# Kernel tuning notes

Measured on AMD Instinct MI355X. Metric: run time of the kernel, lower is better.

## Reference

```python
import jax, jax.numpy as jnp
import numpy as np

H = 16
D_MODEL = 1024
D_K = D_MODEL // H
NEG = -1e9


def setup_inputs() -> dict:
    key = jax.random.key(0)
    ks = jax.random.split(key, 12)
    B, S = 2, 2048
    inp = {
        "query": jax.random.normal(ks[0], (B, S, D_MODEL), jnp.float32),
        "key": jax.random.normal(ks[1], (B, S, D_MODEL), jnp.float32),
        "value": jax.random.normal(ks[2], (B, S, D_MODEL), jnp.float32),
        "mask": jnp.ones((B, 1, S), jnp.int32),
    }
    s = 1.0 / np.sqrt(D_MODEL)
    for i, nm in enumerate(["Wq", "Wk", "Wv", "Wo"]):
        inp[nm] = jax.random.normal(ks[3 + i], (D_MODEL, D_MODEL), jnp.float32) * s
        inp["b" + nm[1]] = jax.random.normal(ks[7 + i], (D_MODEL,), jnp.float32) * s
    return inp


def _split_heads(x):
    B, S, _ = x.shape
    return x.reshape(B, S, H, D_K).transpose(0, 2, 1, 3)  # [B,H,S,Dk]


def reference(query, key, value, mask, Wq, bq, Wk, bk, Wv, bv, Wo, bo):
    q = _split_heads(query @ Wq + bq)
    k = _split_heads(key @ Wk + bk)
    v = _split_heads(value @ Wv + bv)
    scores = jnp.einsum("bhqd,bhkd->bhqk", q, k) / jnp.sqrt(jnp.float32(D_K))
    # mask [B,1,Sk] -> broadcast as [B,1,1,Sk]
    scores = jnp.where(mask[:, None, :, :] == 0, NEG, scores)
    attn = jax.nn.softmax(scores, axis=-1)  # dropout is identity in eval mode
    out = jnp.einsum("bhqk,bhkd->bhqd", attn, v)
    B, _, Sq, _ = out.shape
    out = out.transpose(0, 2, 1, 3).reshape(B, Sq, H * D_K)
    return out @ Wo + bo
```

## Files before the change

kernel.cpp:

```cpp
#include <hip/hip_runtime.h>
#include <hip/hip_bf16.h>

typedef __attribute__((ext_vector_type(8))) short short8;
typedef __attribute__((ext_vector_type(4))) float float4v;
typedef __attribute__((ext_vector_type(2))) unsigned int uint2v;
typedef __hip_bfloat16 bf16;

#define MFMA16(a, b, c) __builtin_amdgcn_mfma_f32_16x16x32_bf16((a), (b), (c), 0, 0, 0)

static __device__ __forceinline__ short8 load8(const bf16* p) {
    return *reinterpret_cast<const short8*>(p);
}
static __device__ __forceinline__ unsigned short bfu(float x) {
    union { bf16 b; unsigned short u; } c; c.b = __float2bfloat16(x); return c.u;
}
static __device__ __forceinline__ unsigned pack2(float lo, float hi) {
    return ((unsigned)bfu(hi) << 16) | bfu(lo);
}
static __device__ __forceinline__ short bf_bits(float x) {
    union { bf16 b; short u; } c; c.b = __float2bfloat16(x); return c.u;
}
static __device__ __forceinline__ short8 cvt8(float4 a, float4 b) {
    short8 r;
    r[0] = bf_bits(a.x); r[1] = bf_bits(a.y); r[2] = bf_bits(a.z); r[3] = bf_bits(a.w);
    r[4] = bf_bits(b.x); r[5] = bf_bits(b.y); r[6] = bf_bits(b.z); r[7] = bf_bits(b.w);
    return r;
}

typedef const __attribute__((address_space(1))) unsigned int* gp1;
typedef __attribute__((address_space(3))) unsigned int* lp3;
static __device__ __forceinline__ void async16(const void* g, void* l) {
    __builtin_amdgcn_global_load_lds((gp1)g, (lp3)l, 16, 0, 0);
}

__global__ __launch_bounds__(256) void transpose_qkv(
    const float* __restrict__ Wq, const float* __restrict__ Wk,
    const float* __restrict__ Wv, bf16* __restrict__ out_base)
{
    __shared__ bf16 tile[64][65];
    const float* in = (blockIdx.z == 0) ? Wq : (blockIdx.z == 1) ? Wk : Wv;
    bf16* out = out_base + (size_t)blockIdx.z * 1048576;
    int tx = threadIdx.x, ty = threadIdx.y;
    int bx = blockIdx.x * 64, by = blockIdx.y * 64;
    for (int i = ty; i < 64; i += 4)
        tile[i][tx] = __float2bfloat16(in[(size_t)(by + i) * 1024 + bx + tx]);
    __syncthreads();
    for (int i = ty; i < 64; i += 4)
        out[(size_t)(bx + i) * 1024 + by + tx] = tile[tx][i];
}

__global__ __launch_bounds__(256) void transpose_one(
    const float* __restrict__ in, bf16* __restrict__ out)
{
    __shared__ bf16 tile[64][65];
    int tx = threadIdx.x, ty = threadIdx.y;
    int bx = blockIdx.x * 64, by = blockIdx.y * 64;
    for (int i = ty; i < 64; i += 4)
        tile[i][tx] = __float2bfloat16(in[(size_t)(by + i) * 1024 + bx + tx]);
    __syncthreads();
    for (int i = ty; i < 64; i += 4)
        out[(size_t)(bx + i) * 1024 + by + tx] = tile[tx][i];
}

__global__ __launch_bounds__(256, 3) void qkv_gemm(
    const float* __restrict__ Xq, const float* __restrict__ Xk,
    const float* __restrict__ Xv, const bf16* __restrict__ Wt_all,
    const float* __restrict__ bq, const float* __restrict__ bk,
    const float* __restrict__ bv,
    bf16* __restrict__ outq, bf16* __restrict__ outk, bf16* __restrict__ outv)
{
    __shared__ float As[128 * 64];
    __shared__ bf16  Bs[128 * 64];

    int wg = blockIdx.x;
    int xcd = wg & 7;
    int jj = wg >> 3;
    int grp = xcd * 12 + (jj >> 3);
    int z = grp >> 5;
    int m_blk = grp & 31;
    int n_blk = jj & 7;

    const float* X    = (z == 0) ? Xq : (z == 1) ? Xk : Xv;
    const float* bias = (z == 0) ? bq : (z == 1) ? bk : bv;
    const bf16*  Wt   = Wt_all + (size_t)z * 1048576;
    bf16*        out  = (z == 0) ? outq : (z == 1) ? outk : outv;
    bool vmode = (z == 2);

    int tid = threadIdx.x;
    int w = tid >> 6, lane = tid & 63, l16 = lane & 15, quad = lane >> 4;
    int m_base = m_blk * 128, n_base = n_blk * 128;

    int r4 = lane >> 4, s16 = lane & 15;
    int r8 = lane >> 3, s8 = lane & 7;
    const float* Asrc0 = X + (size_t)(m_base + w * 32 + r4) * 1024 + ((s16 ^ r4) << 2);
    const float* Asrc1 = X + (size_t)(m_base + w * 32 + r4) * 1024 + ((s16 ^ (4 + r4)) << 2);
    const bf16*  Bsrc  = Wt + (size_t)(n_base + w * 32 + r8) * 1024 + ((s8 ^ r8) << 3);

    int wm = (w & 1) * 64, wn = (w >> 1) * 64;
    int sw = l16 & 7;

    float4v zero = {0.f, 0.f, 0.f, 0.f};
    float4v acc[4][4];
    #pragma unroll
    for (int mi = 0; mi < 4; ++mi)
        #pragma unroll
        for (int nj = 0; nj < 4; ++nj) acc[mi][nj] = zero;

    for (int it = 0; it < 16; ++it) {
        int kt = it * 64;
        #pragma unroll
        for (int p = 0; p < 8; ++p) {
            const float* s = ((p & 1) ? Asrc1 : Asrc0) + (size_t)p * 4096 + kt;
            async16(s, (char*)As + (w * 32 + p * 4) * 256);
        }
        #pragma unroll
        for (int p = 0; p < 4; ++p)
            async16(Bsrc + (size_t)p * 8192 + kt, (char*)Bs + (w * 32 + p * 8) * 128);
        __syncthreads();

        #pragma unroll
        for (int kk = 0; kk < 2; ++kk) {
            short8 af[4], bfr[4];
            #pragma unroll
            for (int mi = 0; mi < 4; ++mi) {
                const float* rp = As + (wm + mi * 16 + l16) * 64;
                float4 f0 = *(const float4*)(rp + (((kk * 8 + quad * 2)     ^ sw) << 2));
                float4 f1 = *(const float4*)(rp + (((kk * 8 + quad * 2 + 1) ^ sw) << 2));
                af[mi] = cvt8(f0, f1);
            }
            #pragma unroll
            for (int nj = 0; nj < 4; ++nj) {
                const bf16* rp = Bs + (wn + nj * 16 + l16) * 64;
                bfr[nj] = load8(rp + (((kk * 4 + quad) ^ sw) << 3));
            }
            #pragma unroll
            for (int mi = 0; mi < 4; ++mi)
                #pragma unroll
                for (int nj = 0; nj < 4; ++nj)
                    acc[mi][nj] = MFMA16(af[mi], bfr[nj], acc[mi][nj]);
        }
        __syncthreads();
    }

    float bsv[4];
    #pragma unroll
    for (int nj = 0; nj < 4; ++nj)
        bsv[nj] = bias[n_base + wn + nj * 16 + l16];

    #pragma unroll
    for (int mi = 0; mi < 4; ++mi) {
        #pragma unroll
        for (int nj = 0; nj < 4; ++nj) {
            int n = n_base + wn + nj * 16 + l16;
            int h = n >> 6, dk = n & 63;
            int m0 = m_base + wm + mi * 16 + quad * 4;
            int b = m0 >> 11, s0 = m0 & 2047;
            if (vmode) {
                float v0 = acc[mi][nj][0] + bsv[nj];
                float v1 = acc[mi][nj][1] + bsv[nj];
                float v2 = acc[mi][nj][2] + bsv[nj];
                float v3 = acc[mi][nj][3] + bsv[nj];
                uint2 pv; pv.x = pack2(v0, v1); pv.y = pack2(v2, v3);
                size_t idx = ((size_t)(b * 16 + h) * 64 + dk) * 2048 + s0;
                *reinterpret_cast<uint2*>(out + idx) = pv;
            } else {
                #pragma unroll
                for (int r = 0; r < 4; ++r) {
                    size_t idx = (((size_t)(b * 16 + h) * 2048 + s0 + r) * 64 + dk);
                    out[idx] = __float2bfloat16(acc[mi][nj][r] + bsv[nj]);
                }
            }
        }
    }
}

__global__ __launch_bounds__(256, 2) void out_gemm(
    const bf16* __restrict__ A, const bf16* __restrict__ Wt,
    const float* __restrict__ bias, float* __restrict__ out)
{
    __shared__ bf16 As[128 * 128];
    __shared__ bf16 Bs[64 * 128];

    int wg = blockIdx.x;
    int xcd = wg & 7;
    int jj = wg >> 3;
    int m_blk = xcd * 4 + (jj >> 4);
    int n_blk = jj & 15;

    int tid = threadIdx.x;
    int w = tid >> 6, lane = tid & 63, l16 = lane & 15, quad = lane >> 4;
    int m_base = m_blk * 128, n_base = n_blk * 64;

    int r4 = lane >> 4, s16 = lane & 15;

    int wm = (w & 1) * 64, wn = (w >> 1) * 32;

    float4v zero = {0.f, 0.f, 0.f, 0.f};
    float4v acc[4][2];
    #pragma unroll
    for (int mi = 0; mi < 4; ++mi)
        #pragma unroll
        for (int nj = 0; nj < 2; ++nj) acc[mi][nj] = zero;

    for (int it = 0; it < 8; ++it) {
        int kt = it * 128;
        #pragma unroll
        for (int p = 0; p < 8; ++p) {
            int row = w * 32 + p * 4 + r4;
            const bf16* s = A + (size_t)(m_base + row) * 1024 + kt
                              + ((s16 ^ (row & 15)) << 3);
            async16(s, (char*)As + (w * 32 + p * 4) * 256);
        }
        #pragma unroll
        for (int p = 0; p < 4; ++p) {
            int row = w * 16 + p * 4 + r4;
            const bf16* s = Wt + (size_t)(n_base + row) * 1024 + kt
                              + ((s16 ^ (row & 15)) << 3);
            async16(s, (char*)Bs + (w * 16 + p * 4) * 256);
        }
        __syncthreads();

        #pragma unroll
        for (int kk = 0; kk < 4; ++kk) {
            short8 af[4], bfr[2];
            #pragma unroll
            for (int mi = 0; mi < 4; ++mi) {
                const bf16* rp = As + (wm + mi * 16 + l16) * 128;
                af[mi] = load8(rp + (((kk * 4 + quad) ^ l16) << 3));
            }
            #pragma unroll
            for (int nj = 0; nj < 2; ++nj) {
                const bf16* rp = Bs + (wn + nj * 16 + l16) * 128;
                bfr[nj] = load8(rp + (((kk * 4 + quad) ^ l16) << 3));
            }
            #pragma unroll
            for (int mi = 0; mi < 4; ++mi)
                #pragma unroll
                for (int nj = 0; nj < 2; ++nj)
                    acc[mi][nj] = MFMA16(af[mi], bfr[nj], acc[mi][nj]);
        }
        __syncthreads();
    }

    float bsv[2];
    #pragma unroll
    for (int nj = 0; nj < 2; ++nj)
        bsv[nj] = bias[n_base + wn + nj * 16 + l16];

    #pragma unroll
    for (int mi = 0; mi < 4; ++mi)
        #pragma unroll
        for (int nj = 0; nj < 2; ++nj) {
            int n = n_base + wn + nj * 16 + l16;
            int m0 = m_base + wm + mi * 16 + quad * 4;
            #pragma unroll
            for (int r = 0; r < 4; ++r)
                out[(size_t)(m0 + r) * 1024 + n] = acc[mi][nj][r] + bsv[nj];
        }
}

__global__ __launch_bounds__(512, 4) void attn_fused(
    const bf16* __restrict__ Qm, const bf16* __restrict__ Km,
    const bf16* __restrict__ Vt, const int* __restrict__ mask,
    bf16* __restrict__ Oout)
{
    __shared__ __align__(16) bf16 Kc[2][64 * 64];
    __shared__ __align__(16) bf16 Vc[2][64 * 64];
    __shared__ unsigned long long maskb[32];

    int tid = threadIdx.x;
    int w = tid >> 6, lane = tid & 63, l16 = lane & 15, quad = lane >> 4;
    int wg = blockIdx.x;
    int xcd = wg & 7;
    int jj = wg >> 3;
    int bh = xcd * 4 + (jj >> 4);
    int qg = jj & 15;
    int b = bh >> 4, h = bh & 15;
    int qt = qg * 8 + w;

    const int* mb = mask + b * 2048;
    #pragma unroll
    for (int i = 0; i < 4; ++i) {
        unsigned long long bal = __ballot(mb[w * 256 + i * 64 + lane] != 0);
        if (lane == 0) maskb[w * 4 + i] = bal;
    }

    const bf16* Qb = Qm + ((size_t)bh * 2048 + (size_t)qt * 16) * 64;
    short8 bQ0 = load8(Qb + l16 * 64 + quad * 8);
    short8 bQ1 = load8(Qb + l16 * 64 + 32 + quad * 8);

    int r8 = lane >> 3, s8 = lane & 7;
    const bf16* Ksrc = Km + (size_t)bh * 131072 + (size_t)(w * 8 + r8) * 64 + ((s8 ^ r8) << 3);
    const bf16* Vsrc = Vt + (size_t)bh * 131072 + (size_t)(w * 8 + r8) * 2048 + ((s8 ^ r8) << 3);

    int sw = l16 & 7;

    float4v zero = {0.f, 0.f, 0.f, 0.f};
    float4v Oacc[4];
    #pragma unroll
    for (int g = 0; g < 4; ++g) Oacc[g] = zero;
    float lsum = 0.f;
    const float C = 0.18033688f;

    async16(Ksrc, (char*)&Kc[0][0] + w * 1024);
    async16(Vsrc, (char*)&Vc[0][0] + w * 1024);
    __syncthreads();

    #pragma unroll 2
    for (int it = 0; it < 32; ++it) {
        int cur = it & 1;
        if (it != 31) {
            async16(Ksrc + (size_t)(it + 1) * 4096, (char*)&Kc[cur ^ 1][0] + w * 1024);
            async16(Vsrc + (size_t)(it + 1) * 64,   (char*)&Vc[cur ^ 1][0] + w * 1024);
        }

        unsigned long long m64 = maskb[it];
        bool full = (m64 == ~0ull);
        const bf16* Kb = &Kc[cur][0];
        const bf16* Vb = &Vc[cur][0];

        float4v S[4];
        #pragma unroll
        for (int kj = 0; kj < 4; ++kj) {
            const bf16* kr = Kb + (kj * 16 + l16) * 64;
            short8 a0 = load8(kr + (((0 + quad) ^ sw) << 3));
            short8 a1 = load8(kr + (((4 + quad) ^ sw) << 3));
            float4v s = MFMA16(a0, bQ0, zero);
            s = MFMA16(a1, bQ1, s);
            S[kj] = s;
        }

        unsigned wlo[4], whi[4];
        #pragma unroll
        for (int kj = 0; kj < 4; ++kj) {
            unsigned m4 = (unsigned)(m64 >> (kj * 16 + quad * 4)) & 0xFu;
            float p[4];
            #pragma unroll
            for (int r = 0; r < 4; ++r)
                p[r] = __builtin_amdgcn_exp2f(S[kj][r] * C);
            if (!full) {
                #pragma unroll
                for (int r = 0; r < 4; ++r)
                    p[r] = ((m4 >> r) & 1u) ? p[r] : 0.f;
            }
            lsum += (p[0] + p[1]) + (p[2] + p[3]);
            wlo[kj] = pack2(p[0], p[1]);
            whi[kj] = pack2(p[2], p[3]);
        }

        short8 ap[2];
        #pragma unroll
        for (int m = 0; m < 2; ++m) {
            uint2v sa = __builtin_amdgcn_permlane32_swap(wlo[2 * m], wlo[2 * m + 1], false, false);
            uint2v qa = __builtin_amdgcn_permlane16_swap(sa[0], sa[1], false, false);
            uint2v sb = __builtin_amdgcn_permlane32_swap(whi[2 * m], whi[2 * m + 1], false, false);
            uint2v qb = __builtin_amdgcn_permlane16_swap(sb[0], sb[1], false, false);
            union { short8 s; unsigned u[4]; } t;
            t.u[0] = qa[0];
            t.u[1] = qb[0];
            t.u[2] = qa[1];
            t.u[3] = qb[1];
            ap[m] = t.s;
        }

        #pragma unroll
        for (int g = 0; g < 4; ++g) {
            const bf16* vr = Vb + (g * 16 + l16) * 64;
            short8 v0 = load8(vr + (((0 + quad) ^ sw) << 3));
            short8 v1 = load8(vr + (((4 + quad) ^ sw) << 3));
            Oacc[g] = MFMA16(ap[0], v0, Oacc[g]);
            Oacc[g] = MFMA16(ap[1], v1, Oacc[g]);
        }

        __syncthreads();
    }

    float ls = lsum;
    ls += __shfl_xor(ls, 16, 64);
    ls += __shfl_xor(ls, 32, 64);
    #pragma unroll
    for (int r = 0; r < 4; ++r) {
        float linv = 1.f / __shfl(ls, quad * 4 + r, 64);
        int srow = qt * 16 + quad * 4 + r;
        size_t base = ((size_t)b * 2048 + srow) * 1024 + h * 64;
        #pragma unroll
        for (int g = 0; g < 4; ++g)
            Oout[base + g * 16 + l16] = __float2bfloat16(Oacc[g][r] * linv);
    }
}

extern "C" void kernel_launch(void* const* d_in, const int* in_sizes, int n_in,
                              void* d_out, int out_size, void* d_ws, size_t ws_size,
                              hipStream_t stream) {
    const float* query = (const float*)d_in[0];
    const float* key   = (const float*)d_in[1];
    const float* value = (const float*)d_in[2];
    const int*   mask  = (const int*)d_in[3];
    const float* Wq = (const float*)d_in[4];
    const float* bq = (const float*)d_in[5];
    const float* Wk = (const float*)d_in[6];
    const float* bk = (const float*)d_in[7];
    const float* Wv = (const float*)d_in[8];
    const float* bv = (const float*)d_in[9];
    const float* Wo = (const float*)d_in[10];
    const float* bo = (const float*)d_in[11];

    char* ws = (char*)d_ws;
    const size_t MB = 1024 * 1024;
    bf16* vb     = (bf16*)ws;
    bf16* Wt_all = (bf16*)(ws + 8 * MB);
    bf16* aout   = (bf16*)(ws + 8 * MB);
    bf16* WtO    = (bf16*)ws;
    bf16* qb     = (bf16*)d_out;
    bf16* kb     = (bf16*)((char*)d_out + 8 * MB);
    float* out   = (float*)d_out;

    transpose_qkv<<<dim3(16, 16, 3), dim3(64, 4), 0, stream>>>(Wq, Wk, Wv, Wt_all);

    qkv_gemm<<<dim3(768), 256, 0, stream>>>(
        query, key, value, Wt_all, bq, bk, bv, qb, kb, vb);

    attn_fused<<<dim3(512), 512, 0, stream>>>(qb, kb, vb, mask, aout);

    transpose_one<<<dim3(16, 16), dim3(64, 4), 0, stream>>>(Wo, WtO);

    out_gemm<<<dim3(512), 256, 0, stream>>>(aout, WtO, bo, out);
}
```

Baseline: 241.2 us.

## Load QKV GEMM A operand directly from global, double-buffer B; shrink attention blocks

The QKV projection GEMM stops staging the fp32 activation tile in shared memory. Each lane now reads its A fragments straight from global memory and converts them to bf16 in registers, and the freed LDS double-buffers the bf16 weight tile so the next K-slice is prefetched while the current one is computed. This removes one barrier per iteration and the LDS traffic for A, but A reads now go uncoalesced through L2 and are not shared between the waves that need the same rows. Separately, the attention kernel drops to 256 threads (4 waves) per block and launches twice as many blocks, with each wave loading twice as much K/V, to change occupancy and scheduling granularity.

```diff
diff --git a/kernel.cpp b/kernel.cpp
--- a/kernel.cpp
+++ b/kernel.cpp
@@ -69,8 +69,7 @@
     const float* __restrict__ bv,
     bf16* __restrict__ outq, bf16* __restrict__ outk, bf16* __restrict__ outv)
 {
-    __shared__ float As[128 * 64];
-    __shared__ bf16  Bs[128 * 64];
+    __shared__ bf16 Bs[2][128 * 64];
 
     int wg = blockIdx.x;
     int xcd = wg & 7;
@@ -90,15 +89,14 @@
     int w = tid >> 6, lane = tid & 63, l16 = lane & 15, quad = lane >> 4;
     int m_base = m_blk * 128, n_base = n_blk * 128;
 
-    int r4 = lane >> 4, s16 = lane & 15;
     int r8 = lane >> 3, s8 = lane & 7;
-    const float* Asrc0 = X + (size_t)(m_base + w * 32 + r4) * 1024 + ((s16 ^ r4) << 2);
-    const float* Asrc1 = X + (size_t)(m_base + w * 32 + r4) * 1024 + ((s16 ^ (4 + r4)) << 2);
-    const bf16*  Bsrc  = Wt + (size_t)(n_base + w * 32 + r8) * 1024 + ((s8 ^ r8) << 3);
+    const bf16* Bsrc = Wt + (size_t)(n_base + w * 32 + r8) * 1024 + ((s8 ^ r8) << 3);
 
     int wm = (w & 1) * 64, wn = (w >> 1) * 64;
     int sw = l16 & 7;
 
+    const float* Abase = X + (size_t)(m_base + wm + l16) * 1024 + quad * 8;
+
     float4v zero = {0.f, 0.f, 0.f, 0.f};
     float4v acc[4][4];
     #pragma unroll
@@ -106,38 +104,40 @@
         #pragma unroll
         for (int nj = 0; nj < 4; ++nj) acc[mi][nj] = zero;
 
+    #pragma unroll
+    for (int p = 0; p < 4; ++p)
+        async16(Bsrc + (size_t)p * 8192, (char*)&Bs[0][0] + (w * 32 + p * 8) * 128);
+    __syncthreads();
+
     for (int it = 0; it < 16; ++it) {
+        int cur = it & 1;
         int kt = it * 64;
-        #pragma unroll
-        for (int p = 0; p < 8; ++p) {
-            const float* s = ((p & 1) ? Asrc1 : Asrc0) + (size_t)p * 4096 + kt;
-            async16(s, (char*)As + (w * 32 + p * 4) * 256);
-        }
-        #pragma unroll
-        for (int p = 0; p < 4; ++p)
-            async16(Bsrc + (size_t)p * 8192 + kt, (char*)Bs + (w * 32 + p * 8) * 128);
-        __syncthreads();
-
+        if (it != 15) {
+            #pragma unroll
+            for (int p = 0; p < 4; ++p)
+                async16(Bsrc + (size_t)p * 8192 + kt + 64,
+                        (char*)&Bs[cur ^ 1][0] + (w * 32 + p * 8) * 128);
+        }
+
+        const bf16* Bb = &Bs[cur][0];
         #pragma unroll
         for (int kk = 0; kk < 2; ++kk) {
-            short8 af[4], bfr[4];
+            short8 bfr[4];
+            #pragma unroll
+            for (int nj = 0; nj < 4; ++nj) {
+                const bf16* rp = Bb + (wn + nj * 16 + l16) * 64;
+                bfr[nj] = load8(rp + (((kk * 4 + quad) ^ sw) << 3));
+            }
             #pragma unroll
             for (int mi = 0; mi < 4; ++mi) {
-                const float* rp = As + (wm + mi * 16 + l16) * 64;
-                float4 f0 = *(const float4*)(rp + (((kk * 8 + quad * 2)     ^ sw) << 2));
-                float4 f1 = *(const float4*)(rp + (((kk * 8 + quad * 2 + 1) ^ sw) << 2));
-                af[mi] = cvt8(f0, f1);
-            }
-            #pragma unroll
-            for (int nj = 0; nj < 4; ++nj) {
-                const bf16* rp = Bs + (wn + nj * 16 + l16) * 64;
-                bfr[nj] = load8(rp + (((kk * 4 + quad) ^ sw) << 3));
-            }
-            #pragma unroll
-            for (int mi = 0; mi < 4; ++mi)
+                const float* ap = Abase + (size_t)mi * 16384 + kt + kk * 32;
+                float4 f0 = *(const float4*)(ap);
+                float4 f1 = *(const float4*)(ap + 4);
+                short8 af = cvt8(f0, f1);
                 #pragma unroll
                 for (int nj = 0; nj < 4; ++nj)
-                    acc[mi][nj] = MFMA16(af[mi], bfr[nj], acc[mi][nj]);
+                    acc[mi][nj] = MFMA16(af, bfr[nj], acc[mi][nj]);
+            }
         }
         __syncthreads();
     }
@@ -259,7 +259,7 @@
         }
 }
 
-__global__ __launch_bounds__(512, 4) void attn_fused(
+__global__ __launch_bounds__(256, 4) void attn_fused(
     const bf16* __restrict__ Qm, const bf16* __restrict__ Km,
     const bf16* __restrict__ Vt, const int* __restrict__ mask,
     bf16* __restrict__ Oout)
@@ -273,16 +273,16 @@
     int wg = blockIdx.x;
     int xcd = wg & 7;
     int jj = wg >> 3;
-    int bh = xcd * 4 + (jj >> 4);
-    int qg = jj & 15;
+    int bh = xcd * 4 + (jj >> 5);
+    int qg = jj & 31;
     int b = bh >> 4, h = bh & 15;
-    int qt = qg * 8 + w;
+    int qt = qg * 4 + w;
 
     const int* mb = mask + b * 2048;
     #pragma unroll
-    for (int i = 0; i < 4; ++i) {
-        unsigned long long bal = __ballot(mb[w * 256 + i * 64 + lane] != 0);
-        if (lane == 0) maskb[w * 4 + i] = bal;
+    for (int i = 0; i < 8; ++i) {
+        unsigned long long bal = __ballot(mb[w * 512 + i * 64 + lane] != 0);
+        if (lane == 0) maskb[w * 8 + i] = bal;
     }
 
     const bf16* Qb = Qm + ((size_t)bh * 2048 + (size_t)qt * 16) * 64;
@@ -290,8 +290,8 @@
     short8 bQ1 = load8(Qb + l16 * 64 + 32 + quad * 8);
 
     int r8 = lane >> 3, s8 = lane & 7;
-    const bf16* Ksrc = Km + (size_t)bh * 131072 + (size_t)(w * 8 + r8) * 64 + ((s8 ^ r8) << 3);
-    const bf16* Vsrc = Vt + (size_t)bh * 131072 + (size_t)(w * 8 + r8) * 2048 + ((s8 ^ r8) << 3);
+    const bf16* Ksrc = Km + (size_t)bh * 131072 + (size_t)(w * 16 + r8) * 64 + ((s8 ^ r8) << 3);
+    const bf16* Vsrc = Vt + (size_t)bh * 131072 + (size_t)(w * 16 + r8) * 2048 + ((s8 ^ r8) << 3);
 
     int sw = l16 & 7;
 
@@ -302,16 +302,24 @@
     float lsum = 0.f;
     const float C = 0.18033688f;
 
-    async16(Ksrc, (char*)&Kc[0][0] + w * 1024);
-    async16(Vsrc, (char*)&Vc[0][0] + w * 1024);
+    #pragma unroll
+    for (int p = 0; p < 2; ++p) {
+        async16(Ksrc + (size_t)p * 512,        (char*)&Kc[0][0] + (w * 16 + p * 8) * 128);
+        async16(Vsrc + (size_t)p * 8 * 2048,   (char*)&Vc[0][0] + (w * 16 + p * 8) * 128);
+    }
     __syncthreads();
 
     #pragma unroll 2
     for (int it = 0; it < 32; ++it) {
         int cur = it & 1;
         if (it != 31) {
-            async16(Ksrc + (size_t)(it + 1) * 4096, (char*)&Kc[cur ^ 1][0] + w * 1024);
-            async16(Vsrc + (size_t)(it + 1) * 64,   (char*)&Vc[cur ^ 1][0] + w * 1024);
+            #pragma unroll
+            for (int p = 0; p < 2; ++p) {
+                async16(Ksrc + (size_t)(it + 1) * 4096 + p * 512,
+                        (char*)&Kc[cur ^ 1][0] + (w * 16 + p * 8) * 128);
+                async16(Vsrc + (size_t)(it + 1) * 64 + (size_t)p * 8 * 2048,
+                        (char*)&Vc[cur ^ 1][0] + (w * 16 + p * 8) * 128);
+            }
         }
 
         unsigned long long m64 = maskb[it];
@@ -420,7 +428,7 @@
     qkv_gemm<<<dim3(768), 256, 0, stream>>>(
         query, key, value, Wt_all, bq, bk, bv, qb, kb, vb);
 
-    attn_fused<<<dim3(512), 512, 0, stream>>>(qb, kb, vb, mask, aout);
+    attn_fused<<<dim3(1024), 256, 0, stream>>>(qb, kb, vb, mask, aout);
 
     transpose_one<<<dim3(16, 16), dim3(64, 4), 0, stream>>>(Wo, WtO);
 
```

Measured after the change: 287.1 us. 19.0% more time.

## Process two query tiles per wave in attention to reuse K/V fragments

Applied to the files above, without the earlier changes.

Each wave in the fused attention kernel now handles two 16-row query tiles instead of one. Every K and V fragment read from LDS feeds twice as many MFMAs, and the grid is halved to 256 workgroups. The cost is more registers (launch bounds relaxed to 2 blocks per SM, loop unroll removed) and fewer workgroups than the 256 CUs can absorb for latency hiding.

```diff
diff --git a/kernel.cpp b/kernel.cpp
--- a/kernel.cpp
+++ b/kernel.cpp
@@ -259,7 +259,7 @@
         }
 }
 
-__global__ __launch_bounds__(512, 4) void attn_fused(
+__global__ __launch_bounds__(512, 2) void attn_fused(
     const bf16* __restrict__ Qm, const bf16* __restrict__ Km,
     const bf16* __restrict__ Vt, const int* __restrict__ mask,
     bf16* __restrict__ Oout)
@@ -273,10 +273,10 @@
     int wg = blockIdx.x;
     int xcd = wg & 7;
     int jj = wg >> 3;
-    int bh = xcd * 4 + (jj >> 4);
-    int qg = jj & 15;
+    int bh = xcd * 4 + (jj >> 3);
+    int qg = jj & 7;
     int b = bh >> 4, h = bh & 15;
-    int qt = qg * 8 + w;
+    int qt0 = qg * 16 + w * 2;
 
     const int* mb = mask + b * 2048;
     #pragma unroll
@@ -285,9 +285,13 @@
         if (lane == 0) maskb[w * 4 + i] = bal;
     }
 
-    const bf16* Qb = Qm + ((size_t)bh * 2048 + (size_t)qt * 16) * 64;
-    short8 bQ0 = load8(Qb + l16 * 64 + quad * 8);
-    short8 bQ1 = load8(Qb + l16 * 64 + 32 + quad * 8);
+    short8 bQ[2][2];
+    #pragma unroll
+    for (int qi = 0; qi < 2; ++qi) {
+        const bf16* Qb = Qm + ((size_t)bh * 2048 + (size_t)(qt0 + qi) * 16) * 64;
+        bQ[qi][0] = load8(Qb + l16 * 64 + quad * 8);
+        bQ[qi][1] = load8(Qb + l16 * 64 + 32 + quad * 8);
+    }
 
     int r8 = lane >> 3, s8 = lane & 7;
     const bf16* Ksrc = Km + (size_t)bh * 131072 + (size_t)(w * 8 + r8) * 64 + ((s8 ^ r8) << 3);
@@ -296,17 +300,18 @@
     int sw = l16 & 7;
 
     float4v zero = {0.f, 0.f, 0.f, 0.f};
-    float4v Oacc[4];
-    #pragma unroll
-    for (int g = 0; g < 4; ++g) Oacc[g] = zero;
-    float lsum = 0.f;
+    float4v Oacc[2][4];
+    #pragma unroll
+    for (int qi = 0; qi < 2; ++qi)
+        #pragma unroll
+        for (int g = 0; g < 4; ++g) Oacc[qi][g] = zero;
+    float lsum[2] = {0.f, 0.f};
     const float C = 0.18033688f;
 
     async16(Ksrc, (char*)&Kc[0][0] + w * 1024);
     async16(Vsrc, (char*)&Vc[0][0] + w * 1024);
     __syncthreads();
 
-    #pragma unroll 2
     for (int it = 0; it < 32; ++it) {
         int cur = it & 1;
         if (it != 31) {
@@ -319,48 +324,53 @@
         const bf16* Kb = &Kc[cur][0];
         const bf16* Vb = &Vc[cur][0];
 
-        float4v S[4];
+        float4v S[2][4];
         #pragma unroll
         for (int kj = 0; kj < 4; ++kj) {
             const bf16* kr = Kb + (kj * 16 + l16) * 64;
             short8 a0 = load8(kr + (((0 + quad) ^ sw) << 3));
             short8 a1 = load8(kr + (((4 + quad) ^ sw) << 3));
-            float4v s = MFMA16(a0, bQ0, zero);
-            s = MFMA16(a1, bQ1, s);
-            S[kj] = s;
-        }
-
-        unsigned wlo[4], whi[4];
-        #pragma unroll
-        for (int kj = 0; kj < 4; ++kj) {
-            unsigned m4 = (unsigned)(m64 >> (kj * 16 + quad * 4)) & 0xFu;
-            float p[4];
-            #pragma unroll
-            for (int r = 0; r < 4; ++r)
-                p[r] = __builtin_amdgcn_exp2f(S[kj][r] * C);
-            if (!full) {
+            #pragma unroll
+            for (int qi = 0; qi < 2; ++qi) {
+                float4v s = MFMA16(a0, bQ[qi][0], zero);
+                s = MFMA16(a1, bQ[qi][1], s);
+                S[qi][kj] = s;
+            }
+        }
+
+        short8 ap[2][2];
+        #pragma unroll
+        for (int qi = 0; qi < 2; ++qi) {
+            unsigned wlo[4], whi[4];
+            #pragma unroll
+            for (int kj = 0; kj < 4; ++kj) {
+                unsigned m4 = (unsigned)(m64 >> (kj * 16 + quad * 4)) & 0xFu;
+                float p[4];
                 #pragma unroll
                 for (int r = 0; r < 4; ++r)
-                    p[r] = ((m4 >> r) & 1u) ? p[r] : 0.f;
-            }
-            lsum += (p[0] + p[1]) + (p[2] + p[3]);
-            wlo[kj] = pack2(p[0], p[1]);
-            whi[kj] = pack2(p[2], p[3]);
-        }
-
-        short8 ap[2];
-        #pragma unroll
-        for (int m = 0; m < 2; ++m) {
-            uint2v sa = __builtin_amdgcn_permlane32_swap(wlo[2 * m], wlo[2 * m + 1], false, false);
-            uint2v qa = __builtin_amdgcn_permlane16_swap(sa[0], sa[1], false, false);
-            uint2v sb = __builtin_amdgcn_permlane32_swap(whi[2 * m], whi[2 * m + 1], false, false);
-            uint2v qb = __builtin_amdgcn_permlane16_swap(sb[0], sb[1], false, false);
-            union { short8 s; unsigned u[4]; } t;
-            t.u[0] = qa[0];
-            t.u[1] = qb[0];
-            t.u[2] = qa[1];
-            t.u[3] = qb[1];
-            ap[m] = t.s;
+                    p[r] = __builtin_amdgcn_exp2f(S[qi][kj][r] * C);
+                if (!full) {
+                    #pragma unroll
+                    for (int r = 0; r < 4; ++r)
+                        p[r] = ((m4 >> r) & 1u) ? p[r] : 0.f;
+                }
+                lsum[qi] += (p[0] + p[1]) + (p[2] + p[3]);
+                wlo[kj] = pack2(p[0], p[1]);
+                whi[kj] = pack2(p[2], p[3]);
+            }
+            #pragma unroll
+            for (int m = 0; m < 2; ++m) {
+                uint2v sa = __builtin_amdgcn_permlane32_swap(wlo[2 * m], wlo[2 * m + 1], false, false);
+                uint2v qa = __builtin_amdgcn_permlane16_swap(sa[0], sa[1], false, false);
+                uint2v sb = __builtin_amdgcn_permlane32_swap(whi[2 * m], whi[2 * m + 1], false, false);
+                uint2v qb2 = __builtin_amdgcn_permlane16_swap(sb[0], sb[1], false, false);
+                union { short8 s; unsigned u[4]; } t;
+                t.u[0] = qa[0];
+                t.u[1] = qb2[0];
+                t.u[2] = qa[1];
+                t.u[3] = qb2[1];
+                ap[qi][m] = t.s;
+            }
         }
 
         #pragma unroll
@@ -368,24 +378,30 @@
             const bf16* vr = Vb + (g * 16 + l16) * 64;
             short8 v0 = load8(vr + (((0 + quad) ^ sw) << 3));
             short8 v1 = load8(vr + (((4 + quad) ^ sw) << 3));
-            Oacc[g] = MFMA16(ap[0], v0, Oacc[g]);
-            Oacc[g] = MFMA16(ap[1], v1, Oacc[g]);
+            #pragma unroll
+            for (int qi = 0; qi < 2; ++qi) {
+                Oacc[qi][g] = MFMA16(ap[qi][0], v0, Oacc[qi][g]);
+                Oacc[qi][g] = MFMA16(ap[qi][1], v1, Oacc[qi][g]);
+            }
         }
 
         __syncthreads();
     }
 
-    float ls = lsum;
-    ls += __shfl_xor(ls, 16, 64);
-    ls += __shfl_xor(ls, 32, 64);
-    #pragma unroll
-    for (int r = 0; r < 4; ++r) {
-        float linv = 1.f / __shfl(ls, quad * 4 + r, 64);
-        int srow = qt * 16 + quad * 4 + r;
-        size_t base = ((size_t)b * 2048 + srow) * 1024 + h * 64;
-        #pragma unroll
-        for (int g = 0; g < 4; ++g)
-            Oout[base + g * 16 + l16] = __float2bfloat16(Oacc[g][r] * linv);
+    #pragma unroll
+    for (int qi = 0; qi < 2; ++qi) {
+        float ls = lsum[qi];
+        ls += __shfl_xor(ls, 16, 64);
+        ls += __shfl_xor(ls, 32, 64);
+        #pragma unroll
+        for (int r = 0; r < 4; ++r) {
+            float linv = 1.f / __shfl(ls, quad * 4 + r, 64);
+            int srow = (qt0 + qi) * 16 + quad * 4 + r;
+            size_t base = ((size_t)b * 2048 + srow) * 1024 + h * 64;
+            #pragma unroll
+            for (int g = 0; g < 4; ++g)
+                Oout[base + g * 16 + l16] = __float2bfloat16(Oacc[qi][g][r] * linv);
+        }
     }
 }
 
@@ -420,7 +436,7 @@
     qkv_gemm<<<dim3(768), 256, 0, stream>>>(
         query, key, value, Wt_all, bq, bk, bv, qb, kb, vb);
 
-    attn_fused<<<dim3(512), 512, 0, stream>>>(qb, kb, vb, mask, aout);
+    attn_fused<<<dim3(256), 512, 0, stream>>>(qb, kb, vb, mask, aout);
 
     transpose_one<<<dim3(16, 16), dim3(64, 4), 0, stream>>>(Wo, WtO);
 
```

After: 249.0 us. 1.03x slower.

## Triple-buffer K/V tiles in attention and fold softmax scale into Q projection

Applied to the files above, without the earlier changes.

The attention kernel moves from double to triple buffering of the K/V LDS tiles. It prefetches two tiles ahead and uses explicit vmcnt waits with raw s_barrier in place of __syncthreads, so global loads can overlap more compute. The softmax scale constant is multiplied into Q in the projection epilogue, which removes one multiply per score element in the inner loop. Triple buffering raises LDS use per block, which may lower occupancy. The hand-written waitcnt logic is fragile: if the loads pending before a barrier are counted wrong, the kernel reads stale data.

```diff
diff --git a/kernel.cpp b/kernel.cpp
--- a/kernel.cpp
+++ b/kernel.cpp
@@ -146,6 +146,8 @@
     #pragma unroll
     for (int nj = 0; nj < 4; ++nj)
         bsv[nj] = bias[n_base + wn + nj * 16 + l16];
+
+    float qs = (z == 0) ? 0.18033688f : 1.0f;
 
     #pragma unroll
     for (int mi = 0; mi < 4; ++mi) {
@@ -167,7 +169,7 @@
                 #pragma unroll
                 for (int r = 0; r < 4; ++r) {
                     size_t idx = (((size_t)(b * 16 + h) * 2048 + s0 + r) * 64 + dk);
-                    out[idx] = __float2bfloat16(acc[mi][nj][r] + bsv[nj]);
+                    out[idx] = __float2bfloat16((acc[mi][nj][r] + bsv[nj]) * qs);
                 }
             }
         }
@@ -264,8 +266,8 @@
     const bf16* __restrict__ Vt, const int* __restrict__ mask,
     bf16* __restrict__ Oout)
 {
-    __shared__ __align__(16) bf16 Kc[2][64 * 64];
-    __shared__ __align__(16) bf16 Vc[2][64 * 64];
+    __shared__ __align__(16) bf16 Kc[3][64 * 64];
+    __shared__ __align__(16) bf16 Vc[3][64 * 64];
     __shared__ unsigned long long maskb[32];
 
     int tid = threadIdx.x;
@@ -300,18 +302,20 @@
     #pragma unroll
     for (int g = 0; g < 4; ++g) Oacc[g] = zero;
     float lsum = 0.f;
-    const float C = 0.18033688f;
-
-    async16(Ksrc, (char*)&Kc[0][0] + w * 1024);
-    async16(Vsrc, (char*)&Vc[0][0] + w * 1024);
-    __syncthreads();
-
-    #pragma unroll 2
+
+    async16(Ksrc,        (char*)&Kc[0][0] + w * 1024);
+    async16(Vsrc,        (char*)&Vc[0][0] + w * 1024);
+    async16(Ksrc + 4096, (char*)&Kc[1][0] + w * 1024);
+    async16(Vsrc + 64,   (char*)&Vc[1][0] + w * 1024);
+    asm volatile("s_waitcnt vmcnt(2) lgkmcnt(0)" ::: "memory");
+    __builtin_amdgcn_s_barrier();
+    __builtin_amdgcn_sched_barrier(0);
+
+    int cur = 0, sb = 2;
     for (int it = 0; it < 32; ++it) {
-        int cur = it & 1;
-        if (it != 31) {
-            async16(Ksrc + (size_t)(it + 1) * 4096, (char*)&Kc[cur ^ 1][0] + w * 1024);
-            async16(Vsrc + (size_t)(it + 1) * 64,   (char*)&Vc[cur ^ 1][0] + w * 1024);
+        if (it < 30) {
+            async16(Ksrc + (size_t)(it + 2) * 4096, (char*)&Kc[sb][0] + w * 1024);
+            async16(Vsrc + (size_t)(it + 2) * 64,   (char*)&Vc[sb][0] + w * 1024);
         }
 
         unsigned long long m64 = maskb[it];
@@ -337,7 +341,7 @@
             float p[4];
             #pragma unroll
             for (int r = 0; r < 4; ++r)
-                p[r] = __builtin_amdgcn_exp2f(S[kj][r] * C);
+                p[r] = __builtin_amdgcn_exp2f(S[kj][r]);
             if (!full) {
                 #pragma unroll
                 for (int r = 0; r < 4; ++r)
@@ -353,13 +357,13 @@
         for (int m = 0; m < 2; ++m) {
             uint2v sa = __builtin_amdgcn_permlane32_swap(wlo[2 * m], wlo[2 * m + 1], false, false);
             uint2v qa = __builtin_amdgcn_permlane16_swap(sa[0], sa[1], false, false);
-            uint2v sb = __builtin_amdgcn_permlane32_swap(whi[2 * m], whi[2 * m + 1], false, false);
-            uint2v qb = __builtin_amdgcn_permlane16_swap(sb[0], sb[1], false, false);
+            uint2v sb2 = __builtin_amdgcn_permlane32_swap(whi[2 * m], whi[2 * m + 1], false, false);
+            uint2v qb2 = __builtin_amdgcn_permlane16_swap(sb2[0], sb2[1], false, false);
             union { short8 s; unsigned u[4]; } t;
             t.u[0] = qa[0];
-            t.u[1] = qb[0];
+            t.u[1] = qb2[0];
             t.u[2] = qa[1];
-            t.u[3] = qb[1];
+            t.u[3] = qb2[1];
             ap[m] = t.s;
         }
 
@@ -372,7 +376,17 @@
             Oacc[g] = MFMA16(ap[1], v1, Oacc[g]);
         }
 
-        __syncthreads();
+        if (it < 30) {
+            asm volatile("s_waitcnt vmcnt(2)" ::: "memory");
+            __builtin_amdgcn_s_barrier();
+            __builtin_amdgcn_sched_barrier(0);
+        } else if (it == 30) {
+            asm volatile("s_waitcnt vmcnt(0)" ::: "memory");
+            __builtin_amdgcn_s_barrier();
+            __builtin_amdgcn_sched_barrier(0);
+        }
+        cur = (cur == 2) ? 0 : cur + 1;
+        sb  = (sb  == 2) ? 0 : sb + 1;
     }
 
     float ls = lsum;
```

Result: no change. 239.5 us (-0.7%).
